# Optimization experiments

Measured on AMD Instinct MI355X. Metric: run time of the kernel, lower is better.

Reference implementation:

```python
import jax, jax.numpy as jnp
import numpy as np

H, D, DS, CZ, S, B = 16, 24, 384, 128, 512, 1
EPS = 1e-5


def setup_inputs() -> dict:
    key = jax.random.key(0)
    ks = jax.random.split(key, 12)
    sc = lambda fan: 1.0 / np.sqrt(fan)
    inp = {
        's': jax.random.normal(ks[0], (B, S, DS), jnp.float32),
        'z': jax.random.normal(ks[1], (B, S, S, CZ), jnp.float32),
        'seq_mask': jnp.zeros((B, 1, 1, S), jnp.float32),
        'q_w': jax.random.normal(ks[2], (H * D, DS), jnp.float32) * sc(DS),
        'q_b': jax.random.normal(ks[3], (H * D,), jnp.float32) * 0.02,
        'k_w': jax.random.normal(ks[4], (H * D, DS), jnp.float32) * sc(DS),
        'v_w': jax.random.normal(ks[5], (H * D, DS), jnp.float32) * sc(DS),
        'g_w': jax.random.normal(ks[6], (H * D, DS), jnp.float32) * sc(DS),
        'o_w': jax.random.normal(ks[7], (DS, H * D), jnp.float32) * sc(H * D),
        'z_ln_w': jnp.ones((CZ,), jnp.float32),
        'z_ln_b': jnp.zeros((CZ,), jnp.float32),
        'z_w': jax.random.normal(ks[8], (H, CZ), jnp.float32) * sc(CZ),
    }
    return inp


def _layer_norm(x, w, b):
    mu = jnp.mean(x, axis=-1, keepdims=True)
    var = jnp.mean(jnp.square(x - mu), axis=-1, keepdims=True)
    return (x - mu) * jax.lax.rsqrt(var + EPS) * w + b


def reference(s, z, seq_mask, q_w, q_b, k_w, v_w, g_w, o_w, z_ln_w, z_ln_b, z_w):
    b, n, _ = s.shape
    # fused QKV projection (q has bias, k/v do not)
    q = (s @ q_w.T + q_b).reshape(b, n, H, D).transpose(0, 2, 1, 3)  # [B,H,S,D]
    k = (s @ k_w.T).reshape(b, n, H, D).transpose(0, 2, 1, 3)
    v = (s @ v_w.T).reshape(b, n, H, D).transpose(0, 2, 1, 3)
    # pair bias: layernorm(z) -> linear to H -> permute to [B,H,S,S]
    bias = _layer_norm(z, z_ln_w, z_ln_b) @ z_w.T          # [B,S,S,H]
    bias = bias.transpose(0, 3, 1, 2)                      # [B,H,S,S]
    bias = bias + seq_mask
    scores = jnp.einsum('bhqd,bhkd->bhqk', q, k) * (D ** -0.5) + bias
    attn = jax.nn.softmax(scores, axis=-1)
    o = jnp.einsum('bhqk,bhkd->bhqd', attn, v)             # [B,H,S,D]
    o = o.transpose(0, 2, 1, 3).reshape(b, n, H * D)
    g = jax.nn.sigmoid(s @ g_w.T)                          # gating
    return (o * g) @ o_w.T                                 # [B,S,DS]
```

## Files before the change

kernel.cpp:

```cpp
#include <hip/hip_runtime.h>

#define H 16
#define D 24
#define DS 384
#define CZ 128
#define S 512
#define EPSV 1e-5f

__global__ __launch_bounds__(256) void proj_kernel(
    const float* __restrict__ s, const float* __restrict__ q_w, const float* __restrict__ q_b,
    const float* __restrict__ k_w, const float* __restrict__ v_w, const float* __restrict__ g_w,
    float* __restrict__ Q, float* __restrict__ K, float* __restrict__ VT, float* __restrict__ G)
{
    const int b = blockIdx.x;
    const int mat = b / 48;
    const int t = b % 48;
    const int by = t / 6, bx = t % 6;
    const float* w = (mat == 0) ? q_w : (mat == 1) ? k_w : (mat == 2) ? v_w : g_w;

    __shared__ float As[32][68];
    __shared__ float Ws[32][68];

    const int tid = threadIdx.x;
    const int tx = tid & 15, ty = tid >> 4;
    const int r8 = tid >> 3;
    const int c4 = tid & 7;

    float acc[4][4] = {};
    for (int kc = 0; kc < DS; kc += 32) {
        __syncthreads();
#pragma unroll
        for (int pass = 0; pass < 2; ++pass) {
            int r = r8 + pass * 32;
            float4 sv = *(const float4*)(s + (by * 64 + r) * DS + kc + c4 * 4);
            float4 wv = *(const float4*)(w + (bx * 64 + r) * DS + kc + c4 * 4);
            As[c4 * 4 + 0][r] = sv.x; As[c4 * 4 + 1][r] = sv.y;
            As[c4 * 4 + 2][r] = sv.z; As[c4 * 4 + 3][r] = sv.w;
            Ws[c4 * 4 + 0][r] = wv.x; Ws[c4 * 4 + 1][r] = wv.y;
            Ws[c4 * 4 + 2][r] = wv.z; Ws[c4 * 4 + 3][r] = wv.w;
        }
        __syncthreads();
#pragma unroll
        for (int k = 0; k < 32; ++k) {
            float4 a4 = *(const float4*)&As[k][ty * 4];
            float4 b4 = *(const float4*)&Ws[k][tx * 4];
            acc[0][0] += a4.x * b4.x; acc[0][1] += a4.x * b4.y; acc[0][2] += a4.x * b4.z; acc[0][3] += a4.x * b4.w;
            acc[1][0] += a4.y * b4.x; acc[1][1] += a4.y * b4.y; acc[1][2] += a4.y * b4.z; acc[1][3] += a4.y * b4.w;
            acc[2][0] += a4.z * b4.x; acc[2][1] += a4.z * b4.y; acc[2][2] += a4.z * b4.z; acc[2][3] += a4.z * b4.w;
            acc[3][0] += a4.w * b4.x; acc[3][1] += a4.w * b4.y; acc[3][2] += a4.w * b4.z; acc[3][3] += a4.w * b4.w;
        }
    }

    const int r0 = by * 64 + ty * 4;
    const int c0 = bx * 64 + tx * 4;
    if (mat == 2) {
#pragma unroll
        for (int ii = 0; ii < 4; ++ii)
#pragma unroll
            for (int jj = 0; jj < 4; ++jj)
                VT[(c0 + jj) * S + (r0 + ii)] = acc[ii][jj];
    } else {
        float* dst = (mat == 0) ? Q : (mat == 1) ? K : G;
#pragma unroll
        for (int ii = 0; ii < 4; ++ii) {
            float4 v;
            v.x = acc[ii][0]; v.y = acc[ii][1]; v.z = acc[ii][2]; v.w = acc[ii][3];
            if (mat == 0) {
                v.x += q_b[c0 + 0]; v.y += q_b[c0 + 1]; v.z += q_b[c0 + 2]; v.w += q_b[c0 + 3];
            } else if (mat == 3) {
                v.x = 1.f / (1.f + __expf(-v.x)); v.y = 1.f / (1.f + __expf(-v.y));
                v.z = 1.f / (1.f + __expf(-v.z)); v.w = 1.f / (1.f + __expf(-v.w));
            }
            *(float4*)(dst + (r0 + ii) * DS + c0) = v;
        }
    }
}

__global__ __launch_bounds__(256) void score_kernel(
    const float* __restrict__ z, const float* __restrict__ seq_mask,
    const float* __restrict__ z_ln_w, const float* __restrict__ z_ln_b,
    const float* __restrict__ z_w,
    const float* __restrict__ Q, const float* __restrict__ K,
    float* __restrict__ scores)
{
    const int b = blockIdx.x;
    const int q = b >> 1;
    const int j0 = (b & 1) * 256;
    const int tid = threadIdx.x;
    const int w = tid >> 6;
    const int lane = tid & 63;
    const int h0 = w * 4;

    __shared__ float a_s[H][CZ + 4];
    __shared__ float AhBh[2][H];
    __shared__ float qrow[DS];
    __shared__ float buf[H][260];

    {
        const int h = tid >> 4;
        const int c8 = (tid & 15) * 8;
        float A = 0.f, Bv = 0.f;
#pragma unroll
        for (int p = 0; p < 2; ++p) {
            float4 wz = *(const float4*)(z_w + h * CZ + c8 + p * 4);
            float4 lw = *(const float4*)(z_ln_w + c8 + p * 4);
            float4 lb = *(const float4*)(z_ln_b + c8 + p * 4);
            float4 a;
            a.x = lw.x * wz.x; a.y = lw.y * wz.y; a.z = lw.z * wz.z; a.w = lw.w * wz.w;
            *(float4*)&a_s[h][c8 + p * 4] = a;
            A += a.x + a.y + a.z + a.w;
            Bv += lb.x * wz.x + lb.y * wz.y + lb.z * wz.z + lb.w * wz.w;
        }
#pragma unroll
        for (int m = 1; m < 16; m <<= 1) {
            A += __shfl_xor(A, m);
            Bv += __shfl_xor(Bv, m);
        }
        if ((tid & 15) == 0) { AhBh[0][h] = A; AhBh[1][h] = Bv; }
    }
    for (int i = tid; i < DS; i += 256) qrow[i] = Q[q * DS + i];
    __syncthreads();

    float accz[4][4];
    float s1[4], s2[4];
#pragma unroll
    for (int i = 0; i < 4; ++i)
#pragma unroll
        for (int bt = 0; bt < 4; ++bt) accz[i][bt] = 0.f;
#pragma unroll
    for (int bt = 0; bt < 4; ++bt) { s1[bt] = 0.f; s2[bt] = 0.f; }

    const float* zq = z + ((long)q * S + j0) * CZ;

    for (int cc = 0; cc < 8; ++cc) {
        const int c0 = cc * 16;
        float4 areg[4][4];
#pragma unroll
        for (int i = 0; i < 4; ++i)
#pragma unroll
            for (int t = 0; t < 4; ++t)
                areg[i][t] = *(const float4*)&a_s[h0 + i][c0 + t * 4];

#pragma unroll
        for (int bt = 0; bt < 4; ++bt) {
            const int row = bt * 64 + lane;
            const float4* zp = (const float4*)(zq + (long)row * CZ + c0);
            float4 zf[4];
#pragma unroll
            for (int t = 0; t < 4; ++t) zf[t] = zp[t];
#pragma unroll
            for (int t = 0; t < 4; ++t) {
                s1[bt] += zf[t].x + zf[t].y + zf[t].z + zf[t].w;
                s2[bt] += zf[t].x * zf[t].x + zf[t].y * zf[t].y
                        + zf[t].z * zf[t].z + zf[t].w * zf[t].w;
            }
#pragma unroll
            for (int i = 0; i < 4; ++i) {
                float a = 0.f;
#pragma unroll
                for (int t = 0; t < 4; ++t)
                    a += zf[t].x * areg[i][t].x + zf[t].y * areg[i][t].y
                       + zf[t].z * areg[i][t].z + zf[t].w * areg[i][t].w;
                accz[i][bt] += a;
            }
        }
    }

    float qk[4][4];
#pragma unroll
    for (int i = 0; i < 4; ++i) {
        const int h = h0 + i;
        float4 qreg[6];
#pragma unroll
        for (int t = 0; t < 6; ++t) qreg[t] = *(const float4*)&qrow[h * D + t * 4];
#pragma unroll
        for (int bt = 0; bt < 4; ++bt) {
            const int row = bt * 64 + lane;
            const float4* kp = (const float4*)(K + (long)(j0 + row) * DS + h * D);
            float a = 0.f;
#pragma unroll
            for (int t = 0; t < 6; ++t) {
                float4 kv = kp[t];
                a += kv.x * qreg[t].x + kv.y * qreg[t].y + kv.z * qreg[t].z + kv.w * qreg[t].w;
            }
            qk[i][bt] = a;
        }
    }

    const float scale = 0.2041241452319315f;
#pragma unroll
    for (int bt = 0; bt < 4; ++bt) {
        const int row = bt * 64 + lane;
        const float mu = s1[bt] * (1.f / 128.f);
        const float rs = rsqrtf(s2[bt] * (1.f / 128.f) - mu * mu + EPSV);
        const float mk = seq_mask[j0 + row];
#pragma unroll
        for (int i = 0; i < 4; ++i) {
            const int h = h0 + i;
            const float bias = rs * accz[i][bt] - mu * rs * AhBh[0][h] + AhBh[1][h];
            buf[h][row] = qk[i][bt] * scale + bias + mk;
        }
    }
    __syncthreads();

#pragma unroll
    for (int it = 0; it < 4; ++it) {
        const int idx = it * 256 + tid;
        const int h = idx >> 6, j4 = idx & 63;
        float4 v = *(const float4*)&buf[h][j4 * 4];
        *(float4*)(scores + ((q << 4) + h) * S + j0 + j4 * 4) = v;
    }
}

__global__ __launch_bounds__(256) void spv_kernel(
    const float* __restrict__ scores, const float* __restrict__ VT,
    const float* __restrict__ G, float* __restrict__ og)
{
    const int q = blockIdx.x;
    const int tid = threadIdx.x;
    const int wv = tid >> 6;
    const int lane = tid & 63;

    __shared__ float sc[H][S + 4];
    __shared__ float opart[4][DS];
    __shared__ float inv_l[H];

    for (int i = tid; i < H * (S / 4); i += 256) {
        int row = i >> 7, f4 = i & 127;
        float4 v = ((const float4*)(scores + ((q << 4) + row) * S))[f4];
        *(float4*)&sc[row][f4 * 4] = v;
    }
    __syncthreads();

#pragma unroll
    for (int i = 0; i < 4; ++i) {
        int h = wv * 4 + i;
        float m = -1e30f;
        for (int j = lane; j < S; j += 64) m = fmaxf(m, sc[h][j]);
#pragma unroll
        for (int mk = 1; mk < 64; mk <<= 1) m = fmaxf(m, __shfl_xor(m, mk));
        float sum = 0.f;
        for (int j = lane; j < S; j += 64) {
            float p = __expf(sc[h][j] - m);
            sc[h][j] = p;
            sum += p;
        }
#pragma unroll
        for (int mk = 1; mk < 64; mk <<= 1) sum += __shfl_xor(sum, mk);
        if (lane == 0) inv_l[h] = 1.f / sum;
    }
    __syncthreads();

#pragma unroll
    for (int ii = 0; ii < 6; ++ii) {
        int idx = ii * 64 + lane;
        int h = idx / 24;
        float acc = 0.f;
        const float4* vt4 = (const float4*)(VT + idx * S + wv * 128);
        const float4* sc4 = (const float4*)&sc[h][wv * 128];
#pragma unroll
        for (int t = 0; t < 32; ++t) {
            float4 p = sc4[t];
            float4 v = vt4[t];
            acc += p.x * v.x + p.y * v.y + p.z * v.z + p.w * v.w;
        }
        opart[wv][idx] = acc;
    }
    __syncthreads();
    for (int i = tid; i < DS; i += 256) {
        float o = opart[0][i] + opart[1][i] + opart[2][i] + opart[3][i];
        int h = i / 24;
        og[q * DS + i] = o * inv_l[h] * G[q * DS + i];
    }
}

__global__ __launch_bounds__(256) void out_kernel(
    const float* __restrict__ og, const float* __restrict__ o_w, float* __restrict__ out)
{
    const int b = blockIdx.x;
    const int by = b / 6, bx = b % 6;

    __shared__ float As[32][68];
    __shared__ float Ws[32][68];

    const int tid = threadIdx.x;
    const int tx = tid & 15, ty = tid >> 4;
    const int r8 = tid >> 3;
    const int c4 = tid & 7;

    float acc[4][4] = {};
    for (int kc = 0; kc < DS; kc += 32) {
        __syncthreads();
#pragma unroll
        for (int pass = 0; pass < 2; ++pass) {
            int r = r8 + pass * 32;
            float4 sv = *(const float4*)(og + (by * 64 + r) * DS + kc + c4 * 4);
            float4 wvv = *(const float4*)(o_w + (bx * 64 + r) * DS + kc + c4 * 4);
            As[c4 * 4 + 0][r] = sv.x; As[c4 * 4 + 1][r] = sv.y;
            As[c4 * 4 + 2][r] = sv.z; As[c4 * 4 + 3][r] = sv.w;
            Ws[c4 * 4 + 0][r] = wvv.x; Ws[c4 * 4 + 1][r] = wvv.y;
            Ws[c4 * 4 + 2][r] = wvv.z; Ws[c4 * 4 + 3][r] = wvv.w;
        }
        __syncthreads();
#pragma unroll
        for (int k = 0; k < 32; ++k) {
            float4 a4 = *(const float4*)&As[k][ty * 4];
            float4 b4 = *(const float4*)&Ws[k][tx * 4];
            acc[0][0] += a4.x * b4.x; acc[0][1] += a4.x * b4.y; acc[0][2] += a4.x * b4.z; acc[0][3] += a4.x * b4.w;
            acc[1][0] += a4.y * b4.x; acc[1][1] += a4.y * b4.y; acc[1][2] += a4.y * b4.z; acc[1][3] += a4.y * b4.w;
            acc[2][0] += a4.z * b4.x; acc[2][1] += a4.z * b4.y; acc[2][2] += a4.z * b4.z; acc[2][3] += a4.z * b4.w;
            acc[3][0] += a4.w * b4.x; acc[3][1] += a4.w * b4.y; acc[3][2] += a4.w * b4.z; acc[3][3] += a4.w * b4.w;
        }
    }

    const int r0 = by * 64 + ty * 4;
    const int c0 = bx * 64 + tx * 4;
#pragma unroll
    for (int ii = 0; ii < 4; ++ii) {
        float4 v;
        v.x = acc[ii][0]; v.y = acc[ii][1]; v.z = acc[ii][2]; v.w = acc[ii][3];
        *(float4*)(out + (r0 + ii) * DS + c0) = v;
    }
}

extern "C" void kernel_launch(void* const* d_in, const int* in_sizes, int n_in,
                              void* d_out, int out_size, void* d_ws, size_t ws_size,
                              hipStream_t stream)
{
    const float* s      = (const float*)d_in[0];
    const float* z      = (const float*)d_in[1];
    const float* mask   = (const float*)d_in[2];
    const float* q_w    = (const float*)d_in[3];
    const float* q_b    = (const float*)d_in[4];
    const float* k_w    = (const float*)d_in[5];
    const float* v_w    = (const float*)d_in[6];
    const float* g_w    = (const float*)d_in[7];
    const float* o_w    = (const float*)d_in[8];
    const float* z_ln_w = (const float*)d_in[9];
    const float* z_ln_b = (const float*)d_in[10];
    const float* z_w    = (const float*)d_in[11];

    float* Q  = (float*)d_ws;
    float* K  = Q + S * DS;
    float* VT = K + S * DS;
    float* G  = VT + S * DS;
    float* og = G + S * DS;
    float* scores = og + S * DS;

    hipLaunchKernelGGL(proj_kernel, dim3(192), dim3(256), 0, stream,
                       s, q_w, q_b, k_w, v_w, g_w, Q, K, VT, G);
    hipLaunchKernelGGL(score_kernel, dim3(S * 2), dim3(256), 0, stream,
                       z, mask, z_ln_w, z_ln_b, z_w, Q, K, scores);
    hipLaunchKernelGGL(spv_kernel, dim3(S), dim3(256), 0, stream,
                       scores, VT, G, og);
    hipLaunchKernelGGL(out_kernel, dim3(48), dim3(256), 0, stream,
                       og, o_w, (float*)d_out);
}
```

Baseline: 396.0 us.

## Stage z tiles through LDS with coalesced loads and split score blocks finer

```diff
diff --git a/kernel.cpp b/kernel.cpp
--- a/kernel.cpp
+++ b/kernel.cpp
@@ -84,8 +84,8 @@
     float* __restrict__ scores)
 {
     const int b = blockIdx.x;
-    const int q = b >> 1;
-    const int j0 = (b & 1) * 256;
+    const int q = b >> 2;
+    const int j0 = (b & 3) * 128;
     const int tid = threadIdx.x;
     const int w = tid >> 6;
     const int lane = tid & 63;
@@ -94,7 +94,7 @@
     __shared__ float a_s[H][CZ + 4];
     __shared__ float AhBh[2][H];
     __shared__ float qrow[DS];
-    __shared__ float buf[H][260];
+    __shared__ float zs[128 * 36];
 
     {
         const int h = tid >> 4;
@@ -119,54 +119,63 @@
         if ((tid & 15) == 0) { AhBh[0][h] = A; AhBh[1][h] = Bv; }
     }
     for (int i = tid; i < DS; i += 256) qrow[i] = Q[q * DS + i];
-    __syncthreads();
-
-    float accz[4][4];
-    float s1[4], s2[4];
-#pragma unroll
-    for (int i = 0; i < 4; ++i)
-#pragma unroll
-        for (int bt = 0; bt < 4; ++bt) accz[i][bt] = 0.f;
-#pragma unroll
-    for (int bt = 0; bt < 4; ++bt) { s1[bt] = 0.f; s2[bt] = 0.f; }
+
+    float accz[4][2];
+    float s1[2] = {0.f, 0.f}, s2[2] = {0.f, 0.f};
+#pragma unroll
+    for (int i = 0; i < 4; ++i) { accz[i][0] = 0.f; accz[i][1] = 0.f; }
 
     const float* zq = z + ((long)q * S + j0) * CZ;
 
-    for (int cc = 0; cc < 8; ++cc) {
-        const int c0 = cc * 16;
-        float4 areg[4][4];
-#pragma unroll
-        for (int i = 0; i < 4; ++i)
-#pragma unroll
-            for (int t = 0; t < 4; ++t)
-                areg[i][t] = *(const float4*)&a_s[h0 + i][c0 + t * 4];
-
-#pragma unroll
-        for (int bt = 0; bt < 4; ++bt) {
-            const int row = bt * 64 + lane;
-            const float4* zp = (const float4*)(zq + (long)row * CZ + c0);
-            float4 zf[4];
-#pragma unroll
-            for (int t = 0; t < 4; ++t) zf[t] = zp[t];
-#pragma unroll
-            for (int t = 0; t < 4; ++t) {
-                s1[bt] += zf[t].x + zf[t].y + zf[t].z + zf[t].w;
-                s2[bt] += zf[t].x * zf[t].x + zf[t].y * zf[t].y
-                        + zf[t].z * zf[t].z + zf[t].w * zf[t].w;
+    for (int st = 0; st < 4; ++st) {
+        const int c0 = st * 32;
+        __syncthreads();
+#pragma unroll
+        for (int it = 0; it < 4; ++it) {
+            const int idx = it * 256 + tid;
+            const int row = idx >> 3, fg = idx & 7;
+            float4 v = *(const float4*)(zq + (long)row * CZ + c0 + fg * 4);
+            *(float4*)&zs[row * 36 + fg * 4] = v;
+        }
+        __syncthreads();
+
+#pragma unroll
+        for (int ccl = 0; ccl < 2; ++ccl) {
+            const int cb = ccl * 16;
+            float4 areg[4][4];
+#pragma unroll
+            for (int i = 0; i < 4; ++i)
+#pragma unroll
+                for (int t = 0; t < 4; ++t)
+                    areg[i][t] = *(const float4*)&a_s[h0 + i][c0 + cb + t * 4];
+
+#pragma unroll
+            for (int bt = 0; bt < 2; ++bt) {
+                const int row = bt * 64 + lane;
+                float4 zf[4];
+#pragma unroll
+                for (int t = 0; t < 4; ++t)
+                    zf[t] = *(const float4*)&zs[row * 36 + cb + t * 4];
+#pragma unroll
+                for (int t = 0; t < 4; ++t) {
+                    s1[bt] += zf[t].x + zf[t].y + zf[t].z + zf[t].w;
+                    s2[bt] += zf[t].x * zf[t].x + zf[t].y * zf[t].y
+                            + zf[t].z * zf[t].z + zf[t].w * zf[t].w;
+                }
+#pragma unroll
+                for (int i = 0; i < 4; ++i) {
+                    float a = 0.f;
+#pragma unroll
+                    for (int t = 0; t < 4; ++t)
+                        a += zf[t].x * areg[i][t].x + zf[t].y * areg[i][t].y
+                           + zf[t].z * areg[i][t].z + zf[t].w * areg[i][t].w;
+                    accz[i][bt] += a;
+                }
             }
-#pragma unroll
-            for (int i = 0; i < 4; ++i) {
-                float a = 0.f;
-#pragma unroll
-                for (int t = 0; t < 4; ++t)
-                    a += zf[t].x * areg[i][t].x + zf[t].y * areg[i][t].y
-                       + zf[t].z * areg[i][t].z + zf[t].w * areg[i][t].w;
-                accz[i][bt] += a;
-            }
-        }
-    }
-
-    float qk[4][4];
+        }
+    }
+
+    float qk[4][2];
 #pragma unroll
     for (int i = 0; i < 4; ++i) {
         const int h = h0 + i;
@@ -174,7 +183,7 @@
 #pragma unroll
         for (int t = 0; t < 6; ++t) qreg[t] = *(const float4*)&qrow[h * D + t * 4];
 #pragma unroll
-        for (int bt = 0; bt < 4; ++bt) {
+        for (int bt = 0; bt < 2; ++bt) {
             const int row = bt * 64 + lane;
             const float4* kp = (const float4*)(K + (long)(j0 + row) * DS + h * D);
             float a = 0.f;
@@ -187,9 +196,11 @@
         }
     }
 
+    __syncthreads();
+    float* buf = zs;
     const float scale = 0.2041241452319315f;
 #pragma unroll
-    for (int bt = 0; bt < 4; ++bt) {
+    for (int bt = 0; bt < 2; ++bt) {
         const int row = bt * 64 + lane;
         const float mu = s1[bt] * (1.f / 128.f);
         const float rs = rsqrtf(s2[bt] * (1.f / 128.f) - mu * mu + EPSV);
@@ -198,16 +209,16 @@
         for (int i = 0; i < 4; ++i) {
             const int h = h0 + i;
             const float bias = rs * accz[i][bt] - mu * rs * AhBh[0][h] + AhBh[1][h];
-            buf[h][row] = qk[i][bt] * scale + bias + mk;
-        }
-    }
-    __syncthreads();
-
-#pragma unroll
-    for (int it = 0; it < 4; ++it) {
+            buf[h * 132 + row] = qk[i][bt] * scale + bias + mk;
+        }
+    }
+    __syncthreads();
+
+#pragma unroll
+    for (int it = 0; it < 2; ++it) {
         const int idx = it * 256 + tid;
-        const int h = idx >> 6, j4 = idx & 63;
-        float4 v = *(const float4*)&buf[h][j4 * 4];
+        const int h = idx >> 5, j4 = idx & 31;
+        float4 v = *(const float4*)&buf[h * 132 + j4 * 4];
         *(float4*)(scores + ((q << 4) + h) * S + j0 + j4 * 4) = v;
     }
 }
@@ -349,7 +360,7 @@
 
     hipLaunchKernelGGL(proj_kernel, dim3(192), dim3(256), 0, stream,
                        s, q_w, q_b, k_w, v_w, g_w, Q, K, VT, G);
-    hipLaunchKernelGGL(score_kernel, dim3(S * 2), dim3(256), 0, stream,
+    hipLaunchKernelGGL(score_kernel, dim3(S * 4), dim3(256), 0, stream,
                        z, mask, z_ln_w, z_ln_b, z_w, Q, K, scores);
     hipLaunchKernelGGL(spv_kernel, dim3(S), dim3(256), 0, stream,
                        scores, VT, G, og);
```

After: 420.5 us. 6.2% more time.
